# Kernel tuning notes

Measured on AMD Instinct MI355X. Metric: run time of the kernel, lower is better.

## Reference

```python
import jax, jax.numpy as jnp
import numpy as np

H, MEL, ATT, TXT = 1024, 80, 640, 640   # n_hidden, n_mel, n_attn_channels, n_text+n_speaker
T, TTXT = 600, 128


def setup_inputs() -> dict:
    key = jax.random.key(0)
    ks = jax.random.split(key, 20)
    def w(k, shape, s=0.02):
        return (jax.random.normal(k, shape) * s).astype(jnp.float32)
    return {
        "residual": jax.random.normal(ks[0], (T, 1, MEL), jnp.float32),
        "text": jax.random.normal(ks[1], (TTXT, 1, TXT), jnp.float32),
        # attention_lstm: LSTM(MEL -> H), 1 layer
        "Wih_a": w(ks[2], (4 * H, MEL)), "Whh_a": w(ks[3], (4 * H, H)),
        "bih_a": jnp.zeros(4 * H, jnp.float32), "bhh_a": jnp.zeros(4 * H, jnp.float32),
        # Attention: query/key/value projections + scoring vector v
        "Wq": w(ks[4], (ATT, H)), "Wk": w(ks[5], (ATT, TXT)), "Wv": w(ks[6], (ATT, TXT)),
        "v_w": w(ks[7], (ATT,)),
        # decoder lstm: LSTM(H+ATT -> H), 2 layers
        "Wih0": w(ks[8], (4 * H, H + ATT)), "Whh0": w(ks[9], (4 * H, H)),
        "bih0": jnp.zeros(4 * H, jnp.float32), "bhh0": jnp.zeros(4 * H, jnp.float32),
        "Wih1": w(ks[10], (4 * H, H)), "Whh1": w(ks[11], (4 * H, H)),
        "bih1": jnp.zeros(4 * H, jnp.float32), "bhh1": jnp.zeros(4 * H, jnp.float32),
        # DenseLayer: two tanh(Linear(H,H))
        "D0w": w(ks[12], (H, H)), "D0b": jnp.zeros(H, jnp.float32),
        "D1w": w(ks[13], (H, H)), "D1b": jnp.zeros(H, jnp.float32),
        # Conv1d(H, 2*MEL, kernel=1) == Linear
        "conv_w": w(ks[14], (2 * MEL, H)), "conv_b": jnp.zeros(2 * MEL, jnp.float32),
        # gate layer: Linear(H+ATT, 1)
        "gate_w": w(ks[15], (H + ATT,)), "gate_b": jnp.zeros((), jnp.float32),
    }


def lstm_cell(x, h, c, Wih, Whh, bih, bhh):
    # PyTorch gate order: i, f, g, o
    g = Wih @ x + bih + Whh @ h + bhh
    i, f, gg, o = jnp.split(g, 4)
    c2 = jax.nn.sigmoid(f) * c + jax.nn.sigmoid(i) * jnp.tanh(gg)
    return jax.nn.sigmoid(o) * jnp.tanh(c2), c2


def ar_back_step(residual, text, Wih_a, Whh_a, bih_a, bhh_a, Wq, Wk, Wv, v_w,
                 Wih0, Whh0, bih0, bhh0, Wih1, Whh1, bih1, bhh1,
                 D0w, D0b, D1w, D1b, conv_w, conv_b, gate_w, gate_b):
    res = residual[::-1, 0, :]            # AR_Back_Step flips time; batch=1 squeezed
    txt = text[:, 0, :]                   # [TTXT, TXT]
    K = txt @ Wk.T                        # [TTXT, ATT]  (keys constant over steps)
    V = txt @ Wv.T                        # [TTXT, ATT]
    z = jnp.zeros(H, jnp.float32)
    carry0 = (jnp.zeros(MEL, jnp.float32), z, z, z, z, z, z)

    def step(carry, r_t):
        out_prev, h, c, h0, c0, h1, c1 = carry
        # attention LSTM on previous output
        h, c = lstm_cell(out_prev, h, c, Wih_a, Whh_a, bih_a, bhh_a)
        # additive (Bahdanau-style) attention: v . tanh(q + K)
        q = Wq @ h                                   # [ATT]
        scores = jnp.tanh(q[None, :] + K) @ v_w      # [TTXT]
        attn = jax.nn.softmax(scores)
        ctx = attn @ V                               # [ATT]
        dec_in = jnp.concatenate([h, ctx])           # [H+ATT]
        # 2-layer decoder LSTM
        h0, c0 = lstm_cell(dec_in, h0, c0, Wih0, Whh0, bih0, bhh0)
        h1, c1 = lstm_cell(h0, h1, c1, Wih1, Whh1, bih1, bhh1)
        # DenseLayer (tanh MLP) then 1x1 conv
        d = jnp.tanh(D1w @ jnp.tanh(D0w @ h1 + D0b) + D1b)
        dec_out = conv_w @ d + conv_b                # [2*MEL]
        log_s, b = dec_out[:MEL], dec_out[MEL:]
        out = (r_t - b) / jnp.exp(log_s)             # affine coupling inverse
        gate = jax.nn.sigmoid(gate_w @ dec_in + gate_b)
        return (out, h, c, h0, c0, h1, c1), (out, gate)

    _, (outs, gates) = jax.lax.scan(step, carry0, res)
    total = outs[::-1][:, None, :]                   # flip back, restore batch dim
    return total, gates


def reference(residual, text, Wih_a, Whh_a, bih_a, bhh_a, Wq, Wk, Wv, v_w,
              Wih0, Whh0, bih0, bhh0, Wih1, Whh1, bih1, bhh1,
              D0w, D0b, D1w, D1b, conv_w, conv_b, gate_w, gate_b):
    return ar_back_step(residual, text, Wih_a, Whh_a, bih_a, bhh_a, Wq, Wk, Wv, v_w,
                        Wih0, Whh0, bih0, bhh0, Wih1, Whh1, bih1, bhh1,
                        D0w, D0b, D1w, D1b, conv_w, conv_b, gate_w, gate_b)
```

## Files before the change

### kernel.cpp

```cpp
#include <hip/hip_runtime.h>

#define NBLK 256
#define NTHR 1024

constexpr int H = 1024, MEL = 80, ATT = 640, TXTD = 640, T = 600, TTXT = 128;
constexpr int G4 = 4096, DIN = H + ATT;

constexpr int WS_K     = 0;
constexpr int WS_V     = WS_K + TTXT * ATT;
constexpr int WS_HV    = WS_V + TTXT * ATT;
constexpr int WS_H0V   = WS_HV + H;
constexpr int WS_H1V   = WS_H0V + H;
constexpr int WS_Q     = WS_H1V + H;
constexpr int WS_CTX   = WS_Q + ATT;
constexpr int WS_DEN   = WS_CTX + ATT;
constexpr int WS_GH    = WS_DEN + 1;
constexpr int WS_DEC   = (WS_GH + 1 + 15) & ~15;
constexpr int WS_A0    = (WS_DEC + 2 * MEL + 15) & ~15;
constexpr int WS_END   = WS_A0 + H;
constexpr int WS_BAR   = (WS_END + 63) & ~63;

constexpr int SM_W0  = 0;
constexpr int SM_H   = SM_W0 + 16 * DIN;
constexpr int SM_H0  = SM_H + H;
constexpr int SM_H1  = SM_H0 + H;
constexpr int SM_A0  = SM_H1 + H;
constexpr int SM_ATT = SM_A0 + H;
constexpr int SM_K   = SM_ATT + ATT;
constexpr int SM_V   = SM_K + ATT;
constexpr int SM_VW  = SM_V + ATT;
constexpr int SM_OUT = SM_VW + ATT;
constexpr int SM_DEC = SM_OUT + MEL;
constexpr int SM_RED = SM_DEC + 2 * MEL;
constexpr int SM_D   = SM_RED + 16;
constexpr int SM_DEN = SM_D + 4;
constexpr int SM_CNT = SM_DEN + 1;
constexpr size_t SM_BYTES = ((size_t)SM_CNT * 4 + 255) & ~(size_t)255;

#define KEEP4(v) \
  asm volatile("" : "+v"((v).x), "+v"((v).y), "+v"((v).z), "+v"((v).w))

struct Params {
  const float *residual, *text, *Wih_a, *Whh_a, *bih_a, *bhh_a,
      *Wq, *Wk, *Wv, *v_w, *Wih0, *Whh0, *bih0, *bhh0,
      *Wih1, *Whh1, *bih1, *bhh1, *D0w, *D0b, *D1w, *D1b,
      *conv_w, *conv_b, *gate_w, *gate_b;
  float* out;
  float* ws;
};

__device__ __forceinline__ float sigm(float x) { return 1.0f / (1.0f + __expf(-x)); }
__device__ __forceinline__ float ftanh(float x) {
  x = fminf(15.f, fmaxf(-15.f, x));
  float e = __expf(2.f * x);
  return (e - 1.f) / (e + 1.f);
}

__device__ __forceinline__ float aload(const float* p) {
  return __hip_atomic_load(p, __ATOMIC_RELAXED, __HIP_MEMORY_SCOPE_AGENT);
}
__device__ __forceinline__ void astore(float* p, float v) {
  __hip_atomic_store(p, v, __ATOMIC_RELAXED, __HIP_MEMORY_SCOPE_AGENT);
}

__device__ __forceinline__ void g_arrive(unsigned* bar) {
  asm volatile("s_waitcnt vmcnt(0)" ::: "memory");
  __syncthreads();
  if (threadIdx.x == 0) {
    unsigned* leaf = bar + (blockIdx.x & 15) * 32;
    unsigned o = __hip_atomic_fetch_add(leaf, 1u, __ATOMIC_RELAXED,
                                        __HIP_MEMORY_SCOPE_AGENT);
    if ((o & 15) == 15)
      __hip_atomic_fetch_add(bar + 544, 1u, __ATOMIC_RELAXED,
                             __HIP_MEMORY_SCOPE_AGENT);
  }
}
__device__ __forceinline__ void g_wait(unsigned* bar, unsigned target) {
  if (threadIdx.x == 0) {
    while (__hip_atomic_load(bar + 544, __ATOMIC_RELAXED,
                             __HIP_MEMORY_SCOPE_AGENT) < target)
      __builtin_amdgcn_s_sleep(1);
  }
  __syncthreads();
}

__device__ __forceinline__ float red64(float s) {
#pragma unroll
  for (int off = 32; off; off >>= 1) s += __shfl_xor(s, off, 64);
  return s;
}

__device__ __forceinline__ float dot16pin(float4 w0, float4 w1, float4 w2,
                                          float4 w3, const float* x, int lane) {
  const float4* x4 = (const float4*)x;
  float4 b0 = x4[lane], b1 = x4[lane + 64], b2 = x4[lane + 128],
         b3 = x4[lane + 192];
  float s0 = w0.x * b0.x, s1 = w1.x * b1.x;
  s0 = fmaf(w0.y, b0.y, s0); s1 = fmaf(w1.y, b1.y, s1);
  s0 = fmaf(w0.z, b0.z, s0); s1 = fmaf(w1.z, b1.z, s1);
  s0 = fmaf(w0.w, b0.w, s0); s1 = fmaf(w1.w, b1.w, s1);
  s0 = fmaf(w2.x, b2.x, s0); s1 = fmaf(w3.x, b3.x, s1);
  s0 = fmaf(w2.y, b2.y, s0); s1 = fmaf(w3.y, b3.y, s1);
  s0 = fmaf(w2.z, b2.z, s0); s1 = fmaf(w3.z, b3.z, s1);
  s0 = fmaf(w2.w, b2.w, s0); s1 = fmaf(w3.w, b3.w, s1);
  return s0 + s1;
}

__device__ __forceinline__ float dot16load(const float* w, const float* x,
                                           int lane) {
  const float4* w4 = (const float4*)w;
  const float4* x4 = (const float4*)x;
  float4 a0 = w4[lane], a1 = w4[lane + 64], a2 = w4[lane + 128],
         a3 = w4[lane + 192];
  float4 b0 = x4[lane], b1 = x4[lane + 64], b2 = x4[lane + 128],
         b3 = x4[lane + 192];
  float s0 = a0.x * b0.x, s1 = a1.x * b1.x;
  s0 = fmaf(a0.y, b0.y, s0); s1 = fmaf(a1.y, b1.y, s1);
  s0 = fmaf(a0.z, b0.z, s0); s1 = fmaf(a1.z, b1.z, s1);
  s0 = fmaf(a0.w, b0.w, s0); s1 = fmaf(a1.w, b1.w, s1);
  s0 = fmaf(a2.x, b2.x, s0); s1 = fmaf(a3.x, b3.x, s1);
  s0 = fmaf(a2.y, b2.y, s0); s1 = fmaf(a3.y, b3.y, s1);
  s0 = fmaf(a2.z, b2.z, s0); s1 = fmaf(a3.z, b3.z, s1);
  s0 = fmaf(a2.w, b2.w, s0); s1 = fmaf(a3.w, b3.w, s1);
  return s0 + s1;
}

__device__ __forceinline__ float wave_dot(const float* __restrict__ w,
                                          const float* __restrict__ x,
                                          int n4, int lane) {
  float s = 0.f;
  const float4* w4 = (const float4*)w;
  const float4* x4 = (const float4*)x;
  for (int i = lane; i < n4; i += 64) {
    float4 a = w4[i];
    float4 b = x4[i];
    s = fmaf(a.x, b.x, s);
    s = fmaf(a.y, b.y, s);
    s = fmaf(a.z, b.z, s);
    s = fmaf(a.w, b.w, s);
  }
  return red64(s);
}

__global__ void __launch_bounds__(NTHR, 4) ar_kernel(Params p) {
  const int b = blockIdx.x;
  const int tid = threadIdx.x;
  const int wave = tid >> 6;
  const int lane = tid & 63;
  const int sg = wave >> 2;
  const int wg = wave & 3;
  const int gw = b * 16 + wave;

  float* ws = p.ws;
  float* Kw = ws + WS_K;
  float* Vw = ws + WS_V;
  float* hv = ws + WS_HV;
  float* h0v = ws + WS_H0V;
  float* h1v = ws + WS_H1V;
  float* qv = ws + WS_Q;
  float* ctxa = ws + WS_CTX;
  float* den = ws + WS_DEN;
  float* ghp = ws + WS_GH;
  float* dec = ws + WS_DEC;
  float* a0g = ws + WS_A0;
  unsigned* bar = (unsigned*)(ws + WS_BAR);

  extern __shared__ __align__(16) float smem[];
  float* s_w0 = smem + SM_W0;
  float* s_h = smem + SM_H;
  float* s_h0 = smem + SM_H0;
  float* s_h1 = smem + SM_H1;
  float* s_a0 = smem + SM_A0;
  float* s_att = smem + SM_ATT;
  float* s_k = smem + SM_K;
  float* s_v = smem + SM_V;
  float* s_vw = smem + SM_VW;
  float* s_out = smem + SM_OUT;
  float* s_dec = smem + SM_DEC;
  float* s_red = smem + SM_RED;
  float* s_d = smem + SM_D;
  float* s_den = smem + SM_DEN;

  const int e = 4 * b + sg;
  const int grow = e + wg * H;

  const float4* WA = (const float4*)(p.Whh_a + (size_t)grow * H);
  float4 wa0 = WA[lane], wa1 = WA[lane + 64], wa2 = WA[lane + 128],
         wa3 = WA[lane + 192];
  KEEP4(wa0); KEEP4(wa1); KEEP4(wa2); KEEP4(wa3);
  const float4* W0 = (const float4*)(p.Whh0 + (size_t)grow * H);
  float4 w00 = W0[lane], w01 = W0[lane + 64], w02 = W0[lane + 128],
         w03 = W0[lane + 192];
  KEEP4(w00); KEEP4(w01); KEEP4(w02); KEEP4(w03);
  const float4* W1 = (const float4*)(p.Whh1 + (size_t)grow * H);
  float4 w10 = W1[lane], w11 = W1[lane + 64], w12 = W1[lane + 128],
         w13 = W1[lane + 192];
  KEEP4(w10); KEEP4(w11); KEEP4(w12); KEEP4(w13);
  const float4* WI = (const float4*)(p.Wih1 + (size_t)grow * H);
  float4 wi0 = WI[lane], wi1 = WI[lane + 64], wi2 = WI[lane + 128],
         wi3 = WI[lane + 192];
  KEEP4(wi0); KEEP4(wi1); KEEP4(wi2); KEEP4(wi3);
  float4 wma = make_float4(0.f, 0.f, 0.f, 0.f);
  if (lane < MEL / 4)
    wma = ((const float4*)(p.Wih_a + (size_t)grow * MEL))[lane];
  KEEP4(wma);
  float4 wf = ((const float4*)(p.D0w + (size_t)e * H))[wg * 64 + lane];
  KEEP4(wf);
  float4 wgd = ((const float4*)(p.D1w + (size_t)e * H))[wg * 64 + lane];
  KEEP4(wgd);
  float4 wcv = make_float4(0.f, 0.f, 0.f, 0.f);
  if (tid < 2 * MEL) wcv = ((const float4*)(p.conv_w + (size_t)tid * H))[b];
  KEEP4(wcv);
  const float ba = p.bih_a[grow] + p.bhh_a[grow];
  const float b0s = p.bih0[grow] + p.bhh0[grow];
  const float b1s = p.bih1[grow] + p.bhh1[grow];

  const float* xsrc = nullptr;
  if (gw < ATT) xsrc = p.Wq + (size_t)gw * H;
  else if (gw == ATT) xsrc = p.gate_w;

  {
    const float4* src = (const float4*)(p.Wih0 + (size_t)grow * DIN);
    float4* dst = (float4*)(s_w0 + wave * DIN);
    for (int i = lane; i < DIN / 4; i += 64) dst[i] = src[i];
  }
  for (int i = tid; i < ATT; i += NTHR) s_vw[i] = p.v_w[i];
  s_h[tid] = 0.f;
  s_h0[tid] = 0.f;
  s_h1[tid] = 0.f;

  float c_reg = 0.f, c0_reg = 0.f, c1_reg = 0.f;
  float u0_reg = 0.f, u1_reg = 0.f, w0h_reg = 0.f;

  unsigned bk = 0;

  for (int idx = gw; idx < 2 * TTXT * ATT; idx += NBLK * 16) {
    int isV = idx >= TTXT * ATT;
    int rem = isV ? idx - TTXT * ATT : idx;
    int j = rem / ATT;
    int a = rem - j * ATT;
    const float* wrow = (isV ? p.Wv : p.Wk) + a * TXTD;
    float s = wave_dot(wrow, p.text + j * TXTD, TXTD / 4, lane);
    if (lane == 0) astore(&(isV ? Vw : Kw)[j * ATT + a], s);
  }
  g_arrive(bar); ++bk; g_wait(bar, 16 * bk);
  if (b < TTXT) {
    for (int i = tid; i < ATT; i += NTHR) {
      s_k[i] = aload(&Kw[b * ATT + i]);
      s_v[i] = aload(&Vw[b * ATT + i]);
    }
  }

  for (int t = 0; t < T; ++t) {
    if (tid < 2 * MEL) s_dec[tid] = aload(dec + tid);
    __syncthreads();
    if (tid < MEL) {
      float o = 0.f;
      if (t != 0) {
        float ls = s_dec[tid] + p.conv_b[tid];
        float bb = s_dec[MEL + tid] + p.conv_b[MEL + tid];
        float r = p.residual[(T - t) * MEL + tid];
        o = (r - bb) * __expf(-ls);
        if (b == 0) p.out[(T - t) * MEL + tid] = o;
      }
      s_out[tid] = o;
    }
    __syncthreads();
    {
      float pa = dot16pin(wa0, wa1, wa2, wa3, s_h, lane);
      if (lane < MEL / 4) {
        float4 bm = ((const float4*)s_out)[lane];
        pa = fmaf(wma.x, bm.x, pa);
        pa = fmaf(wma.y, bm.y, pa);
        pa = fmaf(wma.z, bm.z, pa);
        pa = fmaf(wma.w, bm.w, pa);
      }
      pa = red64(pa);
      if (lane == 0) s_red[wave] = pa + ba;
      __syncthreads();
      if (tid < 4) {
        int ee = 4 * b + tid;
        float gi = s_red[tid * 4 + 0], gf = s_red[tid * 4 + 1];
        float gg = s_red[tid * 4 + 2], go = s_red[tid * 4 + 3];
        float c2 = sigm(gf) * c_reg + sigm(gi) * ftanh(gg);
        c_reg = c2;
        astore(&hv[ee], sigm(go) * ftanh(c2));
      }
    }
    g_arrive(bar); ++bk;
    g_wait(bar, 16 * bk);

    s_h[tid] = aload(hv + tid);
    __syncthreads();
    if (xsrc) {
      float q = dot16load(xsrc, s_h, lane);
      q = red64(q);
      if (lane == 0) {
        if (gw < ATT) astore(&qv[gw], q);
        else astore(&ghp[0], q);
      }
    }
    if (b == NBLK - 1) {
      for (int i = tid; i < ATT; i += NTHR) astore(&ctxa[i], 0.f);
      if (tid == 0) astore(den, 0.f);
      for (int i = tid; i < 2 * MEL; i += NTHR) astore(&dec[i], 0.f);
    }
    g_arrive(bar); ++bk;
    w0h_reg = red64(dot16load(s_w0 + wave * DIN, s_h, lane));
    g_wait(bar, 16 * bk);

    if (b < TTXT) {
      if (tid < ATT) s_att[tid] = aload(&qv[tid]);
      __syncthreads();
      float sp = 0.f;
      for (int i = tid; i < ATT; i += NTHR)
        sp += ftanh(s_att[i] + s_k[i]) * s_vw[i];
      sp = red64(sp);
      if (lane == 0) s_red[wave] = sp;
      __syncthreads();
      float sc = 0.f;
#pragma unroll
      for (int k = 0; k < 16; ++k) sc += s_red[k];
      float pj = __expf(sc - 16.f);
      for (int i = tid; i < ATT; i += NTHR)
        atomicAdd(&ctxa[i], pj * s_v[i]);
      if (tid == 0) atomicAdd(den, pj);
    }
    g_arrive(bar); ++bk;
    g_wait(bar, 16 * bk);

    {
      if (tid < ATT) s_att[tid] = aload(&ctxa[tid]);
      if (tid == NTHR - 1) s_den[0] = aload(den);
      __syncthreads();
      const float4* W4 = (const float4*)(s_w0 + wave * DIN + H);
      const float4* X4 = (const float4*)s_att;
      float4 a_ = W4[lane], b_ = X4[lane];
      float4 a2 = W4[lane + 64], b2 = X4[lane + 64];
      float s = a_.x * b_.x;
      s = fmaf(a_.y, b_.y, s); s = fmaf(a_.z, b_.z, s); s = fmaf(a_.w, b_.w, s);
      s = fmaf(a2.x, b2.x, s); s = fmaf(a2.y, b2.y, s);
      s = fmaf(a2.z, b2.z, s); s = fmaf(a2.w, b2.w, s);
      if (lane < 32) {
        float4 a3 = W4[128 + lane], b3 = X4[128 + lane];
        s = fmaf(a3.x, b3.x, s); s = fmaf(a3.y, b3.y, s);
        s = fmaf(a3.z, b3.z, s); s = fmaf(a3.w, b3.w, s);
      }
      s = red64(s);
      float inv = 1.f / s_den[0];
      if (lane == 0) s_red[wave] = s * inv + w0h_reg + u0_reg + b0s;
      __syncthreads();
      if (tid < 4) {
        int ee = 4 * b + tid;
        float gi = s_red[tid * 4 + 0], gf = s_red[tid * 4 + 1];
        float gg = s_red[tid * 4 + 2], go = s_red[tid * 4 + 3];
        float c2 = sigm(gf) * c0_reg + sigm(gi) * ftanh(gg);
        c0_reg = c2;
        astore(&h0v[ee], sigm(go) * ftanh(c2));
      }
    }
    g_arrive(bar); ++bk;
    if (b == 0 && wave == 15) {
      float inv = 1.f / s_den[0];
      float gc = wave_dot(p.gate_w + H, s_att, ATT / 4, lane);
      if (lane == 0) {
        float gh = aload(&ghp[0]);
        p.out[T * MEL + t] = sigm(gh + gc * inv + p.gate_b[0]);
      }
    }
    g_wait(bar, 16 * bk);

    s_h0[tid] = aload(h0v + tid);
    __syncthreads();
    {
      float pe = dot16pin(wi0, wi1, wi2, wi3, s_h0, lane);
      pe = red64(pe);
      if (lane == 0) s_red[wave] = pe + u1_reg + b1s;
      __syncthreads();
      if (tid < 4) {
        int ee = 4 * b + tid;
        float gi = s_red[tid * 4 + 0], gf = s_red[tid * 4 + 1];
        float gg = s_red[tid * 4 + 2], go = s_red[tid * 4 + 3];
        float c2 = sigm(gf) * c1_reg + sigm(gi) * ftanh(gg);
        c1_reg = c2;
        astore(&h1v[ee], sigm(go) * ftanh(c2));
      }
    }
    g_arrive(bar); ++bk;
    u0_reg = red64(dot16pin(w00, w01, w02, w03, s_h0, lane));
    g_wait(bar, 16 * bk);

    s_h1[tid] = aload(h1v + tid);
    __syncthreads();
    {
      float4 x = ((const float4*)s_h1)[wg * 64 + lane];
      float s = wf.x * x.x;
      s = fmaf(wf.y, x.y, s); s = fmaf(wf.z, x.z, s); s = fmaf(wf.w, x.w, s);
      s = red64(s);
      if (lane == 0) s_red[wave] = s;
      __syncthreads();
      if (tid < 4) {
        int r2 = 4 * b + tid;
        float tot = s_red[tid * 4] + s_red[tid * 4 + 1] + s_red[tid * 4 + 2] +
                    s_red[tid * 4 + 3];
        astore(&a0g[r2], ftanh(tot + p.D0b[r2]));
      }
    }
    g_arrive(bar); ++bk;
    u1_reg = red64(dot16pin(w10, w11, w12, w13, s_h1, lane));
    g_wait(bar, 16 * bk);

    s_a0[tid] = aload(a0g + tid);
    __syncthreads();
    {
      float4 x = ((const float4*)s_a0)[wg * 64 + lane];
      float s = wgd.x * x.x;
      s = fmaf(wgd.y, x.y, s); s = fmaf(wgd.z, x.z, s); s = fmaf(wgd.w, x.w, s);
      s = red64(s);
      if (lane == 0) s_red[wave] = s;
      __syncthreads();
      if (tid < 4) {
        int r2 = 4 * b + tid;
        float tot = s_red[tid * 4] + s_red[tid * 4 + 1] + s_red[tid * 4 + 2] +
                    s_red[tid * 4 + 3];
        s_d[tid] = ftanh(tot + p.D1b[r2]);
      }
      __syncthreads();
      if (tid < 2 * MEL) {
        float acc = wcv.x * s_d[0];
        acc = fmaf(wcv.y, s_d[1], acc);
        acc = fmaf(wcv.z, s_d[2], acc);
        acc = fmaf(wcv.w, s_d[3], acc);
        atomicAdd(&dec[tid], acc);
      }
    }
    g_arrive(bar); ++bk;
    g_wait(bar, 16 * bk);
  }

  if (b == 0 && tid < MEL) {
    float ls = aload(&dec[tid]) + p.conv_b[tid];
    float bb = aload(&dec[MEL + tid]) + p.conv_b[MEL + tid];
    float r = p.residual[tid];
    p.out[tid] = (r - bb) * __expf(-ls);
  }
}

extern "C" void kernel_launch(void* const* d_in, const int* in_sizes, int n_in,
                              void* d_out, int out_size, void* d_ws, size_t ws_size,
                              hipStream_t stream) {
  Params hp;
  hp.residual = (const float*)d_in[0];
  hp.text = (const float*)d_in[1];
  hp.Wih_a = (const float*)d_in[2];
  hp.Whh_a = (const float*)d_in[3];
  hp.bih_a = (const float*)d_in[4];
  hp.bhh_a = (const float*)d_in[5];
  hp.Wq = (const float*)d_in[6];
  hp.Wk = (const float*)d_in[7];
  hp.Wv = (const float*)d_in[8];
  hp.v_w = (const float*)d_in[9];
  hp.Wih0 = (const float*)d_in[10];
  hp.Whh0 = (const float*)d_in[11];
  hp.bih0 = (const float*)d_in[12];
  hp.bhh0 = (const float*)d_in[13];
  hp.Wih1 = (const float*)d_in[14];
  hp.Whh1 = (const float*)d_in[15];
  hp.bih1 = (const float*)d_in[16];
  hp.bhh1 = (const float*)d_in[17];
  hp.D0w = (const float*)d_in[18];
  hp.D0b = (const float*)d_in[19];
  hp.D1w = (const float*)d_in[20];
  hp.D1b = (const float*)d_in[21];
  hp.conv_w = (const float*)d_in[22];
  hp.conv_b = (const float*)d_in[23];
  hp.gate_w = (const float*)d_in[24];
  hp.gate_b = (const float*)d_in[25];
  hp.out = (float*)d_out;
  hp.ws = (float*)d_ws;

  hipMemsetAsync((char*)d_ws + (size_t)WS_BAR * sizeof(float), 0, 4096, stream);

  void* args[] = {&hp};
  hipLaunchCooperativeKernel((void*)ar_kernel, dim3(NBLK), dim3(NTHR), args,
                             (uint32_t)SM_BYTES, stream);
}
```

Before: 26.58 ms.

## Precompute W0·V per text position so attention context needs no atomics

Before the time loop, each wave projects its slice of the decoder input weights onto every value vector, giving M[row, j], and block 0 does the same for the gate weights. Each step then publishes only the per-position attention scores instead of atomically accumulating a 640-wide context vector and denominator into global memory. Every block recomputes the softmax weights from 128 scores and combines them with the precomputed M rows. This removes the per-step global atomics and the context zeroing, at the cost of a one-time precompute and extra shared memory.

```diff
diff --git a/kernel.cpp b/kernel.cpp
--- a/kernel.cpp
+++ b/kernel.cpp
@@ -12,8 +12,8 @@
 constexpr int WS_H0V   = WS_HV + H;
 constexpr int WS_H1V   = WS_H0V + H;
 constexpr int WS_Q     = WS_H1V + H;
-constexpr int WS_CTX   = WS_Q + ATT;
-constexpr int WS_DEN   = WS_CTX + ATT;
+constexpr int WS_SV    = WS_Q + ATT;
+constexpr int WS_DEN   = WS_SV + ATT;
 constexpr int WS_GH    = WS_DEN + 1;
 constexpr int WS_DEC   = (WS_GH + 1 + 15) & ~15;
 constexpr int WS_A0    = (WS_DEC + 2 * MEL + 15) & ~15;
@@ -33,8 +33,10 @@
 constexpr int SM_DEC = SM_OUT + MEL;
 constexpr int SM_RED = SM_DEC + 2 * MEL;
 constexpr int SM_D   = SM_RED + 16;
-constexpr int SM_DEN = SM_D + 4;
-constexpr int SM_CNT = SM_DEN + 1;
+constexpr int SM_M   = SM_D + 4;
+constexpr int SM_MG  = SM_M + 16 * TTXT;
+constexpr int SM_SV  = SM_MG + TTXT;
+constexpr int SM_CNT = SM_SV + TTXT;
 constexpr size_t SM_BYTES = ((size_t)SM_CNT * 4 + 255) & ~(size_t)255;
 
 #define KEEP4(v) \
@@ -158,8 +160,7 @@
   float* h0v = ws + WS_H0V;
   float* h1v = ws + WS_H1V;
   float* qv = ws + WS_Q;
-  float* ctxa = ws + WS_CTX;
-  float* den = ws + WS_DEN;
+  float* sv = ws + WS_SV;
   float* ghp = ws + WS_GH;
   float* dec = ws + WS_DEC;
   float* a0g = ws + WS_A0;
@@ -179,7 +180,9 @@
   float* s_dec = smem + SM_DEC;
   float* s_red = smem + SM_RED;
   float* s_d = smem + SM_D;
-  float* s_den = smem + SM_DEN;
+  float* s_m = smem + SM_M;
+  float* s_mg = smem + SM_MG;
+  float* s_sv = smem + SM_SV;
 
   const int e = 4 * b + sg;
   const int grow = e + wg * H;
@@ -250,6 +253,29 @@
       s_v[i] = aload(&Vw[b * ATT + i]);
     }
   }
+  {
+    const float4* wrow = (const float4*)(s_w0 + wave * DIN + H);
+    for (int j = 0; j < TTXT; ++j) {
+      const float4* v4 = (const float4*)(Vw + j * ATT);
+      float s = 0.f;
+      for (int i = lane; i < ATT / 4; i += 64) {
+        float4 a = wrow[i], x = v4[i];
+        s = fmaf(a.x, x.x, s);
+        s = fmaf(a.y, x.y, s);
+        s = fmaf(a.z, x.z, s);
+        s = fmaf(a.w, x.w, s);
+      }
+      s = red64(s);
+      if (lane == 0) s_m[wave * TTXT + j] = s;
+    }
+  }
+  if (b == 0) {
+    for (int j = wave; j < TTXT; j += 16) {
+      float s = wave_dot(p.gate_w + H, Vw + j * ATT, ATT / 4, lane);
+      if (lane == 0) s_mg[j] = s;
+    }
+  }
+  __syncthreads();
 
   for (int t = 0; t < T; ++t) {
     if (tid < 2 * MEL) s_dec[tid] = aload(dec + tid);
@@ -301,8 +327,6 @@
       }
     }
     if (b == NBLK - 1) {
-      for (int i = tid; i < ATT; i += NTHR) astore(&ctxa[i], 0.f);
-      if (tid == 0) astore(den, 0.f);
       for (int i = tid; i < 2 * MEL; i += NTHR) astore(&dec[i], 0.f);
     }
     g_arrive(bar); ++bk;
@@ -318,37 +342,25 @@
       sp = red64(sp);
       if (lane == 0) s_red[wave] = sp;
       __syncthreads();
-      float sc = 0.f;
+      if (tid == 0) {
+        float sc = 0.f;
 #pragma unroll
-      for (int k = 0; k < 16; ++k) sc += s_red[k];
-      float pj = __expf(sc - 16.f);
-      for (int i = tid; i < ATT; i += NTHR)
-        atomicAdd(&ctxa[i], pj * s_v[i]);
-      if (tid == 0) atomicAdd(den, pj);
+        for (int k = 0; k < 16; ++k) sc += s_red[k];
+        astore(&sv[b], sc);
+      }
     }
     g_arrive(bar); ++bk;
     g_wait(bar, 16 * bk);
 
     {
-      if (tid < ATT) s_att[tid] = aload(&ctxa[tid]);
-      if (tid == NTHR - 1) s_den[0] = aload(den);
-      __syncthreads();
-      const float4* W4 = (const float4*)(s_w0 + wave * DIN + H);
-      const float4* X4 = (const float4*)s_att;
-      float4 a_ = W4[lane], b_ = X4[lane];
-      float4 a2 = W4[lane + 64], b2 = X4[lane + 64];
-      float s = a_.x * b_.x;
-      s = fmaf(a_.y, b_.y, s); s = fmaf(a_.z, b_.z, s); s = fmaf(a_.w, b_.w, s);
-      s = fmaf(a2.x, b2.x, s); s = fmaf(a2.y, b2.y, s);
-      s = fmaf(a2.z, b2.z, s); s = fmaf(a2.w, b2.w, s);
-      if (lane < 32) {
-        float4 a3 = W4[128 + lane], b3 = X4[128 + lane];
-        s = fmaf(a3.x, b3.x, s); s = fmaf(a3.y, b3.y, s);
-        s = fmaf(a3.z, b3.z, s); s = fmaf(a3.w, b3.w, s);
-      }
-      s = red64(s);
-      float inv = 1.f / s_den[0];
-      if (lane == 0) s_red[wave] = s * inv + w0h_reg + u0_reg + b0s;
+      if (tid < TTXT) s_sv[tid] = aload(&sv[tid]);
+      __syncthreads();
+      float pa_ = __expf(s_sv[lane] - 16.f);
+      float pb_ = __expf(s_sv[lane + 64] - 16.f);
+      float den_ = red64(pa_ + pb_);
+      float w0c = red64(fmaf(pa_, s_m[wave * TTXT + lane],
+                             pb_ * s_m[wave * TTXT + lane + 64]));
+      if (lane == 0) s_red[wave] = w0c / den_ + w0h_reg + u0_reg + b0s;
       __syncthreads();
       if (tid < 4) {
         int ee = 4 * b + tid;
@@ -361,11 +373,13 @@
     }
     g_arrive(bar); ++bk;
     if (b == 0 && wave == 15) {
-      float inv = 1.f / s_den[0];
-      float gc = wave_dot(p.gate_w + H, s_att, ATT / 4, lane);
+      float pa_ = __expf(s_sv[lane] - 16.f);
+      float pb_ = __expf(s_sv[lane + 64] - 16.f);
+      float den_ = red64(pa_ + pb_);
+      float gc = red64(fmaf(pa_, s_mg[lane], pb_ * s_mg[lane + 64]));
       if (lane == 0) {
         float gh = aload(&ghp[0]);
-        p.out[T * MEL + t] = sigm(gh + gc * inv + p.gate_b[0]);
+        p.out[T * MEL + t] = sigm(gh + gc / den_ + p.gate_b[0]);
       }
     }
     g_wait(bar, 16 * bk);
```

Measured after the change: 25.47 ms. 1.04x faster.
